# Kernel tuning notes

Hardware: AMD Instinct MI355X
Metric: run time of the kernel (lower is better)

## Reference

```python
import jax, jax.numpy as jnp
import numpy as np
import math

B, C, D, H, W = 1, 64, 16, 16, 16
HEADS = 4
HD = C // HEADS  # head_dim = 16


def conv3d(x, w, b, pad):
    # x: [B,C,D,H,W], w: [O,I,kd,kh,kw], pad: (pd,ph,pw)
    y = jax.lax.conv_general_dilated(
        x, w, window_strides=(1, 1, 1),
        padding=[(p, p) for p in pad],
        dimension_numbers=('NCDHW', 'OIDHW', 'NCDHW'))
    return y + b[None, :, None, None, None]


def setup_inputs() -> dict:
    key = jax.random.key(0)
    ks = jax.random.split(key, 10)
    s = 0.02
    return {
        'x': jax.random.normal(ks[0], (B, C, D, H, W), jnp.float32),
        'gamma': jax.random.normal(ks[1], (1,), jnp.float32),
        'w_sp': jax.random.normal(ks[2], (C, C, 1, 3, 3), jnp.float32) * s,
        'b_sp': jax.random.normal(ks[3], (C,), jnp.float32) * s,
        'w_spec': jax.random.normal(ks[4], (C, C, 3, 1, 1), jnp.float32) * s,
        'b_spec': jax.random.normal(ks[5], (C,), jnp.float32) * s,
        'w_qkv': jax.random.normal(ks[6], (3 * C, C, 1, 1, 1), jnp.float32) * s,
        'b_qkv': jax.random.normal(ks[7], (3 * C,), jnp.float32) * s,
        'w_proj': jax.random.normal(ks[8], (C, C, 1, 1, 1), jnp.float32) * s,
        'b_proj': jax.random.normal(ks[9], (C,), jnp.float32) * s,
    }


def _decay_exponent(dtype):
    # Faithful to the torch permute quirk (requires H == W):
    # exponent[i,j,k,m,n,o] = |i-m| + |j-k| + |n-o|
    dd = jnp.abs(jnp.arange(D)[:, None] - jnp.arange(D)[None, :]).astype(dtype)  # [D,D]
    hh = jnp.abs(jnp.arange(H)[:, None] - jnp.arange(H)[None, :]).astype(dtype)  # [H,H]
    ww = jnp.abs(jnp.arange(W)[:, None] - jnp.arange(W)[None, :]).astype(dtype)  # [W,W]
    return (dd[:, None, None, :, None, None]      # i (axis0), m (axis3)
            + hh[None, :, :, None, None, None]    # j (axis1), k (axis2)
            + ww[None, None, None, None, :, :])   # n (axis4), o (axis5)


def _forward(x, gamma, w_sp, b_sp, w_spec, b_spec, w_qkv, b_qkv, w_proj, b_proj):
    x = conv3d(x, w_sp, b_sp, (0, 1, 1))
    x = conv3d(x, w_spec, b_spec, (1, 0, 0))
    qkv = conv3d(x, w_qkv, b_qkv, (0, 0, 0))
    q, k, v = jnp.split(qkv, 3, axis=1)
    rs = lambda t: t.reshape(B, HEADS, HD, D, H, W)
    q, k, v = rs(q), rs(k), rs(v)

    g = jax.nn.sigmoid(gamma[0])
    decay = g ** _decay_exponent(x.dtype)  # [D,H,W,D,W,W] (H==W)

    # attn[b,h,i,j,k,m,n,o]: (i,j,k)=query D,H,W ; (m,n,o)=key D,H,W
    attn = jnp.einsum('bhdijk,bhdmno->bhijkmno', q, k) / math.sqrt(HD)
    attn = jax.nn.softmax(attn * decay, axis=-1)  # softmax over key-W axis o only
    out = jnp.einsum('bhijkmno,bhdmno->bhdijk', attn, v)
    out = out.reshape(B, C, D, H, W)
    return conv3d(out, w_proj, b_proj, (0, 0, 0))


def reference(x, gamma, w_sp, b_sp, w_spec, b_spec, w_qkv, b_qkv, w_proj, b_proj):
    return _forward(x, gamma, w_sp, b_sp, w_spec, b_spec, w_qkv, b_qkv, w_proj, b_proj)
```

## Files before the change

### kernel.cpp

```cpp
#include <hip/hip_runtime.h>
#include <math.h>

#define CN   262144
#define BTP 196
#define PTP 68

typedef __attribute__((ext_vector_type(8))) short short8;
typedef __attribute__((ext_vector_type(4))) short short4v;
typedef __attribute__((ext_vector_type(4))) float float4v;

static __device__ __forceinline__ unsigned short f2bf(float f) {
    union { float f; unsigned u; } v; v.f = f;
    unsigned r = (v.u + 0x7FFFu + ((v.u >> 16) & 1u)) >> 16;
    return (unsigned short)r;
}

static __device__ __forceinline__ void st_u32g(void* p, unsigned v) {
    __hip_atomic_store((unsigned*)p, v, __ATOMIC_RELAXED,
                       __HIP_MEMORY_SCOPE_AGENT);
}
static __device__ __forceinline__ void st_u64g(void* p, unsigned long long v) {
    __hip_atomic_store((unsigned long long*)p, v, __ATOMIC_RELAXED,
                       __HIP_MEMORY_SCOPE_AGENT);
}
static __device__ __forceinline__ void st_f32g(void* p, float v) {
    __hip_atomic_store((float*)p, v, __ATOMIC_RELAXED,
                       __HIP_MEMORY_SCOPE_AGENT);
}

#define BAR_LIMIT (1 << 20)

static __device__ __forceinline__ void grid_bar(int* arrive, int* release, int phase) {
    __syncthreads();
    if (blockIdx.x == 0) {
        if (threadIdx.x < 64) {
            if (threadIdx.x == 0)
                __hip_atomic_store(&arrive[0], phase,
                                   __ATOMIC_RELAXED, __HIP_MEMORY_SCOPE_AGENT);
            int base = (int)threadIdx.x * 8 * 32;
            int z = 0; bool done = false;
            while (!done && z < BAR_LIMIT) {
                int mn = phase;
                #pragma unroll
                for (int q = 0; q < 8; ++q) {
                    int a = __hip_atomic_load(&arrive[base + q * 32],
                                              __ATOMIC_RELAXED, __HIP_MEMORY_SCOPE_AGENT);
                    mn = (a < mn) ? a : mn;
                }
                done = (mn >= phase);
                if (!done) __builtin_amdgcn_s_sleep(1);
                ++z;
            }
            __hip_atomic_store(&release[(int)threadIdx.x * 32], phase,
                               __ATOMIC_RELAXED, __HIP_MEMORY_SCOPE_AGENT);
        }
        __syncthreads();
    } else {
        if (threadIdx.x == 0) {
            __hip_atomic_store(&arrive[(int)blockIdx.x * 32], phase,
                               __ATOMIC_RELAXED, __HIP_MEMORY_SCOPE_AGENT);
            int* rel = &release[(blockIdx.x & 63) * 32];
            int z = 0;
            while (__hip_atomic_load(rel, __ATOMIC_RELAXED,
                                     __HIP_MEMORY_SCOPE_AGENT) < phase
                   && z < BAR_LIMIT) {
                __builtin_amdgcn_s_sleep(2);
                ++z;
            }
        }
        __syncthreads();
    }
}

__global__ __launch_bounds__(512, 4) void mega_kernel(
        const float* __restrict__ x, const float* __restrict__ gamma,
        const float* __restrict__ w_sp, const float* __restrict__ b_sp,
        const float* __restrict__ w_spec, const float* __restrict__ b_spec,
        const float* __restrict__ w_qkv, const float* __restrict__ b_qkv,
        const float* __restrict__ w_proj, const float* __restrict__ b_proj,
        float* __restrict__ out, float* ws, int* arrive, int* release) {
    __shared__ __align__(16) unsigned char lds_raw[32896];

    float* y1  = ws;
    unsigned short* wfb = (unsigned short*)(ws + CN);
    float* bfv = ws + CN + 20480;
    unsigned short* wsb = (unsigned short*)(ws + CN + 24576);
    unsigned short* qb  = (unsigned short*)(ws + 2 * CN);
    unsigned short* kb  = (unsigned short*)(ws + 2 * CN + CN / 2);
    unsigned short* vtb = (unsigned short*)(ws + 3 * CN);
    float* aoall = ws + 3 * CN + CN / 2;

    if (blockIdx.x < 36) {
        int idx2 = blockIdx.x * 512 + threadIdx.x;
        int idx = idx2 * 2;
        int dh  = idx / 12288;
        int rem = idx % 12288;
        int co  = rem / 192;
        int kp  = rem % 192;
        const float* wrow = w_sp + co * 576 + dh * 3;
        unsigned short e0 = f2bf(wrow[(kp / 3) * 9 + (kp % 3)]);
        unsigned short e1 = f2bf(wrow[((kp + 1) / 3) * 9 + ((kp + 1) % 3)]);
        st_u32g(wsb + idx, (unsigned)e0 | ((unsigned)e1 << 16));
    }
    grid_bar(arrive, release, 1);

    if (blockIdx.x < 256) {
        unsigned short* Bt = (unsigned short*)lds_raw;
        int d = blockIdx.x >> 4;
        int h = blockIdx.x & 15;
        int tid = threadIdx.x;
        bool act = tid < 256;
        int px = tid & 15, cig = (tid >> 4) & 15;

        float rcur[12], rnxt[12];
        #define LOAD_CHUNK(dh_, rr)                                            \
            {                                                                  \
                int hh = h + (dh_) - 1;                                        \
                _Pragma("unroll")                                              \
                for (int cc = 0; cc < 4; ++cc) {                               \
                    int ci = cig * 4 + cc;                                     \
                    const float* xr = x + ci * 4096 + d * 256 + hh * 16;       \
                    _Pragma("unroll")                                          \
                    for (int dw = 0; dw < 3; ++dw) {                           \
                        int ww = px + dw - 1;                                  \
                        float v = 0.f;                                         \
                        if (hh >= 0 && hh <= 15 && ww >= 0 && ww <= 15)        \
                            v = xr[ww];                                        \
                        (rr)[cc * 3 + dw] = v;                                 \
                    }                                                          \
                }                                                              \
            }

        if (act) LOAD_CHUNK(0, rcur);

        int wv = (tid >> 6) & 3, lane = tid & 63;
        int quad = lane >> 4, l15 = lane & 15;
        float4v acc = {0.f, 0.f, 0.f, 0.f};

        #pragma unroll
        for (int c = 0; c < 3; ++c) {
            __syncthreads();
            if (act) {
                #pragma unroll
                for (int cc = 0; cc < 4; ++cc) {
                    int ci = cig * 4 + cc;
                    Bt[px * BTP + ci * 3 + 0] = f2bf(rcur[cc * 3 + 0]);
                    Bt[px * BTP + ci * 3 + 1] = f2bf(rcur[cc * 3 + 1]);
                    Bt[px * BTP + ci * 3 + 2] = f2bf(rcur[cc * 3 + 2]);
                }
            }
            __syncthreads();
            if (act) {
                if (c < 2) LOAD_CHUNK(c + 1, rnxt);

                const unsigned short* ab = wsb + c * 12288 + (wv * 16 + l15) * 192 + quad * 8;
                const unsigned short* brow = Bt + l15 * BTP + quad * 8;
                #pragma unroll
                for (int ks = 0; ks < 6; ++ks) {
                    short8 af = *(const short8*)(ab + ks * 32);
                    short4v lo = *(const short4v*)(brow + ks * 32);
                    short4v hi = *(const short4v*)(brow + ks * 32 + 4);
                    short8 bf8 = {lo[0], lo[1], lo[2], lo[3], hi[0], hi[1], hi[2], hi[3]};
                    acc = __builtin_amdgcn_mfma_f32_16x16x32_bf16(af, bf8, acc, 0, 0, 0);
                }
                #pragma unroll
                for (int q2 = 0; q2 < 12; ++q2) rcur[q2] = rnxt[q2];
            }
        }

        if (act) {
            int p = d * 256 + h * 16 + l15;
            #pragma unroll
            for (int r = 0; r < 4; ++r) {
                int co = wv * 16 + quad * 4 + r;
                st_f32g(y1 + co * 4096 + p, acc[r] + b_sp[co]);
            }
        }
        #undef LOAD_CHUNK
    } else {
        int idx = (blockIdx.x - 256) * 512 + threadIdx.x;
        if (idx < 18432) {
            int oc = idx / 96;
            int rp = idx % 96;
            int r0 = rp * 2;
            float s0 = 0.f, s1 = 0.f;
            #pragma unroll 8
            for (int ci = 0; ci < 64; ++ci) {
                float wq = w_qkv[oc * 64 + ci];
                s0 += wq * w_spec[ci * 192 + r0];
                s1 += wq * w_spec[ci * 192 + r0 + 1];
            }
            if (oc < 64) { s0 *= 0.25f; s1 *= 0.25f; }
            st_u32g(wfb + oc * 192 + r0,
                    (unsigned)f2bf(s0) | ((unsigned)f2bf(s1) << 16));
        } else if (idx < 18432 + 192) {
            int j = idx - 18432;
            float t = b_qkv[j];
            for (int ci = 0; ci < 64; ++ci) t += w_qkv[j * 64 + ci] * b_spec[ci];
            if (j < 64) t *= 0.25f;
            st_f32g(bfv + j, t);
        }
    }
    grid_bar(arrive, release, 2);

    if (blockIdx.x < 384) {
        unsigned short* Bt = (unsigned short*)lds_raw;
        int bI  = blockIdx.x;
        int ocg = bI % 3;
        int pq  = (bI / 3) & 7;
        int d   = bI / 24;
        int tid = threadIdx.x;

        {
            int px  = tid & 31;
            int cig = tid >> 5;
            const float* yb = y1 + d * 256 + pq * 32 + px;
            #pragma unroll
            for (int cc = 0; cc < 4; ++cc) {
                int ci = cig * 4 + cc;
                const float* yc = yb + ci * 4096;
                #pragma unroll
                for (int t = 0; t < 3; ++t) {
                    float v = 0.f;
                    if (!((d == 0 && t == 0) || (d == 15 && t == 2)))
                        v = yc[(t - 1) * 256];
                    Bt[px * BTP + ci * 3 + t] = f2bf(v);
                }
            }
        }

        int wv = tid >> 6, lane = tid & 63;
        int quad = lane >> 4, l15 = lane & 15;
        int Mt = wv >> 1;
        int nt = wv & 1;

        short8 af[6];
        {
            const unsigned short* ab = wfb + (ocg * 64 + Mt * 16 + l15) * 192 + quad * 8;
            #pragma unroll
            for (int ks = 0; ks < 6; ++ks) af[ks] = *(const short8*)(ab + ks * 32);
        }
        float bias[4];
        #pragma unroll
        for (int r = 0; r < 4; ++r) bias[r] = bfv[ocg * 64 + Mt * 16 + quad * 4 + r];

        __syncthreads();

        float4v czero = {0.f, 0.f, 0.f, 0.f};
        float4v acc = czero;
        {
            const unsigned short* brow = Bt + (nt * 16 + l15) * BTP + quad * 8;
            #pragma unroll
            for (int ks = 0; ks < 6; ++ks) {
                short4v lo = *(const short4v*)(brow + ks * 32);
                short4v hi = *(const short4v*)(brow + ks * 32 + 4);
                short8 bf8 = {lo[0], lo[1], lo[2], lo[3], hi[0], hi[1], hi[2], hi[3]};
                acc = __builtin_amdgcn_mfma_f32_16x16x32_bf16(af[ks], bf8, acc, 0, 0, 0);
            }
        }

        {
            int p = d * 256 + pq * 32 + nt * 16 + l15;
            if (ocg == 2) {
                int h = (p >> 4) & 15, w0 = p & 15;
                int kap = 8 * (w0 >> 2) + 4 * (h & 1) + (w0 & 3);
                unsigned short* dstb = vtb + ((Mt * 16 + d) * 8 + (h >> 1)) * 512
                                           + (quad * 4) * 32;
                int odd = l15 & 1;
                int kap_e = kap - odd;
                #pragma unroll
                for (int r = 0; r < 4; ++r) {
                    unsigned self = f2bf(acc[r] + bias[r]);
                    unsigned other = (unsigned)__shfl_xor((int)self, 1) & 0xFFFFu;
                    unsigned pk = odd ? (other | (self << 16)) : (self | (other << 16));
                    if ((r < 2) == (odd != 0)) continue;
                    st_u32g(dstb + r * 32 + kap_e, pk);
                }
            } else {
                unsigned short* dst = (ocg == 0 ? qb : kb) + Mt * 65536 + p * 16 + quad * 4;
                unsigned t0 = (unsigned)f2bf(acc[0] + bias[0])
                            | ((unsigned)f2bf(acc[1] + bias[1]) << 16);
                unsigned t1 = (unsigned)f2bf(acc[2] + bias[2])
                            | ((unsigned)f2bf(acc[3] + bias[3]) << 16);
                st_u64g(dst, (unsigned long long)t0 | ((unsigned long long)t1 << 32));
            }
        }
    }
    grid_bar(arrive, release, 3);

    {
        unsigned short* KSH = (unsigned short*)lds_raw;
        float* gp = (float*)(lds_raw + 32768);
        int tid = threadIdx.x;
        int bI = blockIdx.x;
        int head = bI >> 7;
        int mg   = (bI >> 5) & 3;
        int oct  = bI & 31;

        if (tid < 32) {
            float g = 1.f / (1.f + __expf(-gamma[0]));
            gp[tid] = __powf(g, (float)tid);
        }

        int wv = tid >> 6, lane = tid & 63;
        int quad = lane >> 4, l15 = lane & 15;
        int t = oct * 8 + wv;
        int i = t >> 4, j = t & 15;

        short8 zero8 = {0, 0, 0, 0, 0, 0, 0, 0};
        float4v czero = {0.f, 0.f, 0.f, 0.f};
        short8 qf = zero8;
        if (quad < 2)
            qf = *(const short8*)(qb + head * 65536 + (t * 16 + l15) * 16 + quad * 8);

        {
            const float4* kbh = (const float4*)(kb + head * 65536 + mg * 4 * 4096);
            #pragma unroll
            for (int q = 0; q < 4; ++q)
                ((float4*)KSH)[q * 512 + tid] = kbh[q * 512 + tid];
        }
        __syncthreads();

        float wd[4];
        #pragma unroll
        for (int r = 0; r < 4; ++r)
            wd[r] = gp[abs(l15 - (quad * 4 + r))] * 1.4426950408889634f;

        float4v O = czero;
        #pragma unroll 1
        for (int mm = 0; mm < 4; ++mm) {
            int m = mg * 4 + mm;
            const unsigned short* kk = KSH + mm * 4096;
            const unsigned short* vvg = vtb + head * 65536 + m * 4096;
            int eim = abs(i - m);
            #pragma unroll
            for (int np = 0; np < 8; ++np) {
                union { unsigned u[4]; short8 s8; } a2u;
                #pragma unroll
                for (int s = 0; s < 2; ++s) {
                    int n = np * 2 + s;
                    short8 a1 = zero8;
                    if (quad < 2)
                        a1 = *(const short8*)(kk + n * 256 + l15 * 16 + quad * 8);
                    float4v d1 = __builtin_amdgcn_mfma_f32_16x16x32_bf16(a1, qf, czero, 0, 0, 0);
                    float smn = gp[eim + abs(j - n)];
                    float e0 = __builtin_amdgcn_exp2f(d1[0] * smn * wd[0]);
                    float e1 = __builtin_amdgcn_exp2f(d1[1] * smn * wd[1]);
                    float e2 = __builtin_amdgcn_exp2f(d1[2] * smn * wd[2]);
                    float e3 = __builtin_amdgcn_exp2f(d1[3] * smn * wd[3]);
                    float sm = e0 + e1 + e2 + e3;
                    sm += __shfl_xor(sm, 16);
                    sm += __shfl_xor(sm, 32);
                    float inv = __builtin_amdgcn_rcpf(sm);
                    union { float f; unsigned u; } p0, p1, p2, p3;
                    p0.f = e0 * inv; p1.f = e1 * inv;
                    p2.f = e2 * inv; p3.f = e3 * inv;
                    a2u.u[s * 2]     = ((p0.u + 0x8000u) >> 16) | ((p1.u + 0x8000u) & 0xFFFF0000u);
                    a2u.u[s * 2 + 1] = ((p2.u + 0x8000u) >> 16) | ((p3.u + 0x8000u) & 0xFFFF0000u);
                }
                short8 b2 = *(const short8*)(vvg + np * 512 + l15 * 32 + quad * 8);
                O = __builtin_amdgcn_mfma_f32_16x16x32_bf16(a2u.s8, b2, O, 0, 0, 0);
            }
        }

        float* aop = aoall + mg * CN + (head * 16 + l15) * 4096 + t * 16 + quad * 4;
        union { float f[2]; unsigned long long u; } o01, o23;
        o01.f[0] = O[0]; o01.f[1] = O[1];
        o23.f[0] = O[2]; o23.f[1] = O[3];
        st_u64g(aop, o01.u);
        st_u64g(aop + 2, o23.u);
    }
    grid_bar(arrive, release, 4);

    if (blockIdx.x < 256) {
        unsigned short* Bt = (unsigned short*)lds_raw;
        int d   = blockIdx.x >> 4;
        int p16 = blockIdx.x & 15;
        int tid = threadIdx.x;
        bool act = tid < 256;

        if (act) {
            int px = tid & 15, cig = (tid >> 4) & 15;
            int gbase = d * 256 + p16 * 16 + px;
            #pragma unroll
            for (int cc = 0; cc < 4; ++cc) {
                int ci = cig * 4 + cc;
                int ga = ci * 4096 + gbase;
                float v = 0.f;
                #pragma unroll
                for (int k = 0; k < 4; ++k) v += aoall[k * CN + ga];
                Bt[px * PTP + ci] = f2bf(v);
            }
        }
        __syncthreads();

        if (act) {
            int wv = (tid >> 6) & 3, lane = tid & 63;
            int quad = lane >> 4, l15 = lane & 15;
            float4v czero = {0.f, 0.f, 0.f, 0.f};
            float4v acc = czero;

            short8 af[2];
            const float* wsrc = w_proj + (wv * 16 + l15) * 64 + quad * 8;
            #pragma unroll
            for (int ks = 0; ks < 2; ++ks) {
                float4 wa = *(const float4*)(wsrc + ks * 32);
                float4 wb = *(const float4*)(wsrc + ks * 32 + 4);
                short8 a8 = {(short)f2bf(wa.x), (short)f2bf(wa.y), (short)f2bf(wa.z),
                             (short)f2bf(wa.w), (short)f2bf(wb.x), (short)f2bf(wb.y),
                             (short)f2bf(wb.z), (short)f2bf(wb.w)};
                af[ks] = a8;
            }
            const unsigned short* brow = Bt + l15 * PTP + quad * 8;
            #pragma unroll
            for (int ks = 0; ks < 2; ++ks) {
                short4v lo = *(const short4v*)(brow + ks * 32);
                short4v hi = *(const short4v*)(brow + ks * 32 + 4);
                short8 bf8 = {lo[0], lo[1], lo[2], lo[3], hi[0], hi[1], hi[2], hi[3]};
                acc = __builtin_amdgcn_mfma_f32_16x16x32_bf16(af[ks], bf8, acc, 0, 0, 0);
            }

            int p = d * 256 + p16 * 16 + l15;
            #pragma unroll
            for (int r = 0; r < 4; ++r) {
                int oc = wv * 16 + quad * 4 + r;
                out[oc * 4096 + p] = acc[r] + b_proj[oc];
            }
        }
    }
}

extern "C" void kernel_launch(void* const* d_in, const int* in_sizes, int n_in,
                              void* d_out, int out_size, void* d_ws, size_t ws_size,
                              hipStream_t stream) {
    const float* x      = (const float*)d_in[0];
    const float* gamma  = (const float*)d_in[1];
    const float* w_sp   = (const float*)d_in[2];
    const float* b_sp   = (const float*)d_in[3];
    const float* w_spec = (const float*)d_in[4];
    const float* b_spec = (const float*)d_in[5];
    const float* w_qkv  = (const float*)d_in[6];
    const float* b_qkv  = (const float*)d_in[7];
    const float* w_proj = (const float*)d_in[8];
    const float* b_proj = (const float*)d_in[9];
    float* out = (float*)d_out;
    float* ws = (float*)d_ws;

    int* arrive  = (int*)(ws + 12 * CN);
    int* release = arrive + 512 * 32;
    hipMemsetAsync(arrive, 0, (512 + 64) * 128, stream);

    mega_kernel<<<dim3(512), dim3(512), 0, stream>>>(
        x, gamma, w_sp, b_sp, w_spec, b_spec, w_qkv, b_qkv, w_proj, b_proj,
        out, ws, arrive, release);
}
```

Before: 120.7 us.

## Use decentralized grid barrier and producer/consumer warp split in conv stage

The grid barrier drops its central release step: every block now polls all 512 arrive flags with 64 lanes, which removes one round-trip through block 0. The first conv stage gives the idle upper 256 threads a producer role that builds bf16 input chunks into a double-buffered LDS tile while the lower threads run MFMA, replacing the register prefetch. The projection stage's reduction now uses all 512 threads. The risk is more polling traffic on the shared flags from 512 blocks.

Result: slower. 134.9 us (+11.8%).

```diff
diff --git a/kernel.cpp b/kernel.cpp
--- a/kernel.cpp
+++ b/kernel.cpp
@@ -30,46 +30,28 @@
 
 #define BAR_LIMIT (1 << 20)
 
-static __device__ __forceinline__ void grid_bar(int* arrive, int* release, int phase) {
+static __device__ __forceinline__ void grid_bar(int* arrive, int phase) {
     __syncthreads();
-    if (blockIdx.x == 0) {
-        if (threadIdx.x < 64) {
-            if (threadIdx.x == 0)
-                __hip_atomic_store(&arrive[0], phase,
-                                   __ATOMIC_RELAXED, __HIP_MEMORY_SCOPE_AGENT);
-            int base = (int)threadIdx.x * 8 * 32;
-            int z = 0; bool done = false;
-            while (!done && z < BAR_LIMIT) {
-                int mn = phase;
-                #pragma unroll
-                for (int q = 0; q < 8; ++q) {
-                    int a = __hip_atomic_load(&arrive[base + q * 32],
-                                              __ATOMIC_RELAXED, __HIP_MEMORY_SCOPE_AGENT);
-                    mn = (a < mn) ? a : mn;
-                }
-                done = (mn >= phase);
-                if (!done) __builtin_amdgcn_s_sleep(1);
-                ++z;
-            }
-            __hip_atomic_store(&release[(int)threadIdx.x * 32], phase,
-                               __ATOMIC_RELAXED, __HIP_MEMORY_SCOPE_AGENT);
-        }
-        __syncthreads();
-    } else {
-        if (threadIdx.x == 0) {
+    if (threadIdx.x < 64) {
+        if (threadIdx.x == 0)
             __hip_atomic_store(&arrive[(int)blockIdx.x * 32], phase,
                                __ATOMIC_RELAXED, __HIP_MEMORY_SCOPE_AGENT);
-            int* rel = &release[(blockIdx.x & 63) * 32];
-            int z = 0;
-            while (__hip_atomic_load(rel, __ATOMIC_RELAXED,
-                                     __HIP_MEMORY_SCOPE_AGENT) < phase
-                   && z < BAR_LIMIT) {
-                __builtin_amdgcn_s_sleep(2);
-                ++z;
-            }
-        }
-        __syncthreads();
-    }
+        int base = (int)threadIdx.x * 8 * 32;
+        int z = 0; bool done = false;
+        while (!done && z < BAR_LIMIT) {
+            int mn = phase;
+            #pragma unroll
+            for (int q = 0; q < 8; ++q) {
+                int a = __hip_atomic_load(&arrive[base + q * 32],
+                                          __ATOMIC_RELAXED, __HIP_MEMORY_SCOPE_AGENT);
+                mn = (a < mn) ? a : mn;
+            }
+            done = (mn >= phase);
+            if (!done) __builtin_amdgcn_s_sleep(1);
+            ++z;
+        }
+    }
+    __syncthreads();
 }
 
 __global__ __launch_bounds__(512, 4) void mega_kernel(
@@ -78,7 +60,7 @@
         const float* __restrict__ w_spec, const float* __restrict__ b_spec,
         const float* __restrict__ w_qkv, const float* __restrict__ b_qkv,
         const float* __restrict__ w_proj, const float* __restrict__ b_proj,
-        float* __restrict__ out, float* ws, int* arrive, int* release) {
+        float* __restrict__ out, float* ws, int* arrive) {
     __shared__ __align__(16) unsigned char lds_raw[32896];
 
     float* y1  = ws;
@@ -102,18 +84,18 @@
         unsigned short e1 = f2bf(wrow[((kp + 1) / 3) * 9 + ((kp + 1) % 3)]);
         st_u32g(wsb + idx, (unsigned)e0 | ((unsigned)e1 << 16));
     }
-    grid_bar(arrive, release, 1);
+    grid_bar(arrive, 1);
 
     if (blockIdx.x < 256) {
-        unsigned short* Bt = (unsigned short*)lds_raw;
+        unsigned short* Bt0 = (unsigned short*)lds_raw;
+        unsigned short* Bt1 = (unsigned short*)lds_raw + 16 * BTP;
         int d = blockIdx.x >> 4;
         int h = blockIdx.x & 15;
         int tid = threadIdx.x;
-        bool act = tid < 256;
+        bool prod = tid >= 256;
         int px = tid & 15, cig = (tid >> 4) & 15;
 
-        float rcur[12], rnxt[12];
-        #define LOAD_CHUNK(dh_, rr)                                            \
+        #define BUILD_CHUNK(dh_, BT)                                           \
             {                                                                  \
                 int hh = h + (dh_) - 1;                                        \
                 _Pragma("unroll")                                              \
@@ -126,12 +108,12 @@
                         float v = 0.f;                                         \
                         if (hh >= 0 && hh <= 15 && ww >= 0 && ww <= 15)        \
                             v = xr[ww];                                        \
-                        (rr)[cc * 3 + dw] = v;                                 \
+                        (BT)[px * BTP + ci * 3 + dw] = f2bf(v);                \
                     }                                                          \
                 }                                                              \
             }
 
-        if (act) LOAD_CHUNK(0, rcur);
+        if (prod) BUILD_CHUNK(0, Bt0);
 
         int wv = (tid >> 6) & 3, lane = tid & 63;
         int quad = lane >> 4, l15 = lane & 15;
@@ -140,21 +122,12 @@
         #pragma unroll
         for (int c = 0; c < 3; ++c) {
             __syncthreads();
-            if (act) {
-                #pragma unroll
-                for (int cc = 0; cc < 4; ++cc) {
-                    int ci = cig * 4 + cc;
-                    Bt[px * BTP + ci * 3 + 0] = f2bf(rcur[cc * 3 + 0]);
-                    Bt[px * BTP + ci * 3 + 1] = f2bf(rcur[cc * 3 + 1]);
-                    Bt[px * BTP + ci * 3 + 2] = f2bf(rcur[cc * 3 + 2]);
-                }
-            }
-            __syncthreads();
-            if (act) {
-                if (c < 2) LOAD_CHUNK(c + 1, rnxt);
-
+            if (prod) {
+                if (c < 2) BUILD_CHUNK(c + 1, (c & 1) ? Bt0 : Bt1);
+            } else {
+                const unsigned short* Btc = (c & 1) ? Bt1 : Bt0;
                 const unsigned short* ab = wsb + c * 12288 + (wv * 16 + l15) * 192 + quad * 8;
-                const unsigned short* brow = Bt + l15 * BTP + quad * 8;
+                const unsigned short* brow = Btc + l15 * BTP + quad * 8;
                 #pragma unroll
                 for (int ks = 0; ks < 6; ++ks) {
                     short8 af = *(const short8*)(ab + ks * 32);
@@ -163,12 +136,10 @@
                     short8 bf8 = {lo[0], lo[1], lo[2], lo[3], hi[0], hi[1], hi[2], hi[3]};
                     acc = __builtin_amdgcn_mfma_f32_16x16x32_bf16(af, bf8, acc, 0, 0, 0);
                 }
-                #pragma unroll
-                for (int q2 = 0; q2 < 12; ++q2) rcur[q2] = rnxt[q2];
-            }
-        }
-
-        if (act) {
+            }
+        }
+
+        if (!prod) {
             int p = d * 256 + h * 16 + l15;
             #pragma unroll
             for (int r = 0; r < 4; ++r) {
@@ -176,7 +147,7 @@
                 st_f32g(y1 + co * 4096 + p, acc[r] + b_sp[co]);
             }
         }
-        #undef LOAD_CHUNK
+        #undef BUILD_CHUNK
     } else {
         int idx = (blockIdx.x - 256) * 512 + threadIdx.x;
         if (idx < 18432) {
@@ -201,7 +172,7 @@
             st_f32g(bfv + j, t);
         }
     }
-    grid_bar(arrive, release, 2);
+    grid_bar(arrive, 2);
 
     if (blockIdx.x < 384) {
         unsigned short* Bt = (unsigned short*)lds_raw;
@@ -286,7 +257,7 @@
             }
         }
     }
-    grid_bar(arrive, release, 3);
+    grid_bar(arrive, 3);
 
     {
         unsigned short* KSH = (unsigned short*)lds_raw;
@@ -370,21 +341,20 @@
         st_u64g(aop, o01.u);
         st_u64g(aop + 2, o23.u);
     }
-    grid_bar(arrive, release, 4);
+    grid_bar(arrive, 4);
 
     if (blockIdx.x < 256) {
         unsigned short* Bt = (unsigned short*)lds_raw;
         int d   = blockIdx.x >> 4;
         int p16 = blockIdx.x & 15;
         int tid = threadIdx.x;
-        bool act = tid < 256;
-
-        if (act) {
-            int px = tid & 15, cig = (tid >> 4) & 15;
+
+        {
+            int px = tid & 15, cig = tid >> 4;
             int gbase = d * 256 + p16 * 16 + px;
             #pragma unroll
-            for (int cc = 0; cc < 4; ++cc) {
-                int ci = cig * 4 + cc;
+            for (int cc = 0; cc < 2; ++cc) {
+                int ci = cig * 2 + cc;
                 int ga = ci * 4096 + gbase;
                 float v = 0.f;
                 #pragma unroll
@@ -394,7 +364,7 @@
         }
         __syncthreads();
 
-        if (act) {
+        if (tid < 256) {
             int wv = (tid >> 6) & 3, lane = tid & 63;
             int quad = lane >> 4, l15 = lane & 15;
             float4v czero = {0.f, 0.f, 0.f, 0.f};
@@ -446,11 +416,10 @@
     float* out = (float*)d_out;
     float* ws = (float*)d_ws;
 
-    int* arrive  = (int*)(ws + 12 * CN);
-    int* release = arrive + 512 * 32;
-    hipMemsetAsync(arrive, 0, (512 + 64) * 128, stream);
+    int* arrive = (int*)(ws + 12 * CN);
+    hipMemsetAsync(arrive, 0, 512 * 128, stream);
 
     mega_kernel<<<dim3(512), dim3(512), 0, stream>>>(
         x, gamma, w_sp, b_sp, w_spec, b_spec, w_qkv, b_qkv, w_proj, b_proj,
-        out, ws, arrive, release);
-}
+        out, ws, arrive);
+}
```
